# Kernel tuning notes

Measured on AMD Instinct MI355X. Metric: run time of the kernel, lower is better.

## Reference

```python
import jax, jax.numpy as jnp
import numpy as np

D = 4096  # input_dim
H = 4096  # hidden_dim


def setup_inputs() -> dict:
    key = jax.random.key(0)
    k_x, k_w, k_b, k_v, k_c = jax.random.split(key, 5)
    x = jax.random.uniform(k_x, (D, 1), dtype=jnp.float32)  # observed pixel values
    w = jax.random.normal(k_w, (H, D), dtype=jnp.float32) * 0.02
    b = jax.random.normal(k_b, (D, 1), dtype=jnp.float32) * 0.02
    v = jax.random.normal(k_v, (D, H), dtype=jnp.float32) * 0.02
    c = jax.random.normal(k_c, (H, 1), dtype=jnp.float32) * 0.02
    return {"x": x, "w": w, "b": b, "v": v, "c": c}


def reference(x, w, b, v, c):
    # Original loop: a_0 = c; a_{i+1} = a_i + w[:, i] * x[i]
    # => a_i = c + sum_{j < i} w[:, j] * x[j]  (exclusive cumsum of rank-1 updates)
    wx = w * x[:, 0][None, :]                      # [H, D]
    cum = jnp.cumsum(wx, axis=1)                   # inclusive cumsum over columns
    A = c + jnp.pad(cum[:, :-1], ((0, 0), (1, 0)))  # exclusive cumsum -> a_i in column i, [H, D]
    h = jax.nn.sigmoid(A)                          # h_i = sigmoid(a_i), [H, D]
    # p_i = sigmoid(v[i, :] @ h_i + b[i])
    logits = jnp.einsum("ih,hi->i", v, h)[:, None] + b  # [D, 1]
    p_x = jax.nn.sigmoid(logits)                   # [D, 1]
    return p_x
```

## Files before the change

### kernel.cpp

```cpp
#include <hip/hip_runtime.h>
#include <hip/hip_fp16.h>

#define D_DIM 4096
#define H_DIM 4096
#define HB 16
#define BLK 1024
#define NBLK (H_DIM / HB)
#define TILE 512
#define NTL (D_DIM / TILE)

__device__ __forceinline__ float fast_sigmoid(float a) {
    return __builtin_amdgcn_rcpf(1.0f + __expf(-a));
}

__device__ __forceinline__ float2 h2_to_f2(unsigned u) {
    union { unsigned u; __half2 h; } cvt;
    cvt.u = u;
    return __half22float2(cvt.h);
}

template <bool ATOMIC>
__global__ __launch_bounds__(BLK, 4) void nade_main_kernel(
    const float* __restrict__ x,
    const float* __restrict__ w,
    const float* __restrict__ v,
    const float* __restrict__ c,
    float* __restrict__ part)
{
    __shared__ __half S[HB][D_DIM];

    const int tid  = threadIdx.x;
    const int wv   = tid >> 6;
    const int lane = tid & 63;
    const int h0   = blockIdx.x * HB;

    const float* wrow = w + (size_t)(h0 + wv) * D_DIM + 8 * lane;
    float carry = c[h0 + wv];

    float4 wA0 = *reinterpret_cast<const float4*>(wrow + 0 * TILE);
    float4 wA1 = *reinterpret_cast<const float4*>(wrow + 0 * TILE + 4);
    float4 wB0 = *reinterpret_cast<const float4*>(wrow + 1 * TILE);
    float4 wB1 = *reinterpret_cast<const float4*>(wrow + 1 * TILE + 4);

    auto scan_tile = [&](int t, float4 w0, float4 w1) {
        const float* xp = x + t * TILE + 8 * lane;
        float4 x0 = *reinterpret_cast<const float4*>(xp);
        float4 x1 = *reinterpret_cast<const float4*>(xp + 4);
        float p0 = w0.x * x0.x, p1 = w0.y * x0.y, p2 = w0.z * x0.z, p3 = w0.w * x0.w;
        float p4 = w1.x * x1.x, p5 = w1.y * x1.y, p6 = w1.z * x1.z, p7 = w1.w * x1.w;
        float s8 = ((p0 + p1) + (p2 + p3)) + ((p4 + p5) + (p6 + p7));
        float incl = s8;
        #pragma unroll
        for (int off = 1; off < 64; off <<= 1) {
            float tv = __shfl_up(incl, off, 64);
            incl += (lane >= off) ? tv : 0.0f;
        }
        float tot = __shfl(incl, 63, 64);
        float a = carry + incl - s8;
        float sg0 = fast_sigmoid(a); a += p0;
        float sg1 = fast_sigmoid(a); a += p1;
        float sg2 = fast_sigmoid(a); a += p2;
        float sg3 = fast_sigmoid(a); a += p3;
        float sg4 = fast_sigmoid(a); a += p4;
        float sg5 = fast_sigmoid(a); a += p5;
        float sg6 = fast_sigmoid(a); a += p6;
        float sg7 = fast_sigmoid(a);
        carry += tot;
        union { __half2 h2[4]; uint4 u; } P;
        P.h2[0] = __floats2half2_rn(sg0, sg1);
        P.h2[1] = __floats2half2_rn(sg2, sg3);
        P.h2[2] = __floats2half2_rn(sg4, sg5);
        P.h2[3] = __floats2half2_rn(sg6, sg7);
        *reinterpret_cast<uint4*>(&S[wv][t * TILE + 8 * lane]) = P.u;
    };

    scan_tile(0, wA0, wA1);
    wA0 = *reinterpret_cast<const float4*>(wrow + 2 * TILE);
    wA1 = *reinterpret_cast<const float4*>(wrow + 2 * TILE + 4);
    scan_tile(1, wB0, wB1);
    wB0 = *reinterpret_cast<const float4*>(wrow + 3 * TILE);
    wB1 = *reinterpret_cast<const float4*>(wrow + 3 * TILE + 4);
    scan_tile(2, wA0, wA1);
    wA0 = *reinterpret_cast<const float4*>(wrow + 4 * TILE);
    wA1 = *reinterpret_cast<const float4*>(wrow + 4 * TILE + 4);
    scan_tile(3, wB0, wB1);
    wB0 = *reinterpret_cast<const float4*>(wrow + 5 * TILE);
    wB1 = *reinterpret_cast<const float4*>(wrow + 5 * TILE + 4);
    scan_tile(4, wA0, wA1);
    wA0 = *reinterpret_cast<const float4*>(wrow + 6 * TILE);
    wA1 = *reinterpret_cast<const float4*>(wrow + 6 * TILE + 4);
    scan_tile(5, wB0, wB1);
    wB0 = *reinterpret_cast<const float4*>(wrow + 7 * TILE);
    wB1 = *reinterpret_cast<const float4*>(wrow + 7 * TILE + 4);
    scan_tile(6, wA0, wA1);
    scan_tile(7, wB0, wB1);

    __syncthreads();

    const int i0 = 4 * tid;

    uint2 sr[16];
    #pragma unroll
    for (int h = 0; h < 16; ++h)
        sr[h] = *reinterpret_cast<const uint2*>(&S[h][i0]);

    const float* vp = v + (size_t)i0 * H_DIM + h0;
    float acc0 = 0.0f, acc1 = 0.0f, acc2 = 0.0f, acc3 = 0.0f;

    {
        float4 vr0[4], vr1[4];
        #pragma unroll
        for (int k = 0; k < 4; ++k) {
            vr0[k] = *reinterpret_cast<const float4*>(vp + 4 * k);
            vr1[k] = *reinterpret_cast<const float4*>(vp + H_DIM + 4 * k);
        }
        #pragma unroll
        for (int k = 0; k < 4; ++k) {
            float2 f0 = h2_to_f2(sr[4 * k + 0].x);
            float2 f1 = h2_to_f2(sr[4 * k + 1].x);
            float2 f2 = h2_to_f2(sr[4 * k + 2].x);
            float2 f3 = h2_to_f2(sr[4 * k + 3].x);
            acc0 += vr0[k].x * f0.x + vr0[k].y * f1.x + vr0[k].z * f2.x + vr0[k].w * f3.x;
            acc1 += vr1[k].x * f0.y + vr1[k].y * f1.y + vr1[k].z * f2.y + vr1[k].w * f3.y;
        }
    }
    {
        float4 vr2[4], vr3[4];
        #pragma unroll
        for (int k = 0; k < 4; ++k) {
            vr2[k] = *reinterpret_cast<const float4*>(vp + 2 * (size_t)H_DIM + 4 * k);
            vr3[k] = *reinterpret_cast<const float4*>(vp + 3 * (size_t)H_DIM + 4 * k);
        }
        #pragma unroll
        for (int k = 0; k < 4; ++k) {
            float2 f0 = h2_to_f2(sr[4 * k + 0].y);
            float2 f1 = h2_to_f2(sr[4 * k + 1].y);
            float2 f2 = h2_to_f2(sr[4 * k + 2].y);
            float2 f3 = h2_to_f2(sr[4 * k + 3].y);
            acc2 += vr2[k].x * f0.x + vr2[k].y * f1.x + vr2[k].z * f2.x + vr2[k].w * f3.x;
            acc3 += vr3[k].x * f0.y + vr3[k].y * f1.y + vr3[k].z * f2.y + vr3[k].w * f3.y;
        }
    }

    if (ATOMIC) {
        atomicAdd(&part[i0 + 0], acc0);
        atomicAdd(&part[i0 + 1], acc1);
        atomicAdd(&part[i0 + 2], acc2);
        atomicAdd(&part[i0 + 3], acc3);
    } else {
        float4 o; o.x = acc0; o.y = acc1; o.z = acc2; o.w = acc3;
        *reinterpret_cast<float4*>(part + (size_t)blockIdx.x * D_DIM + i0) = o;
    }
}

__global__ __launch_bounds__(1024, 1) void nade_reduce_kernel(
    const float* __restrict__ part,
    const float* __restrict__ b,
    float* __restrict__ out)
{
    __shared__ float red[16][64];
    const int tid = threadIdx.x;
    const int bg  = tid >> 6;
    const int il  = tid & 63;
    const int i   = blockIdx.x * 64 + il;
    float s = 0.0f;
    #pragma unroll
    for (int j = 0; j < NBLK / 16; ++j)
        s += part[(size_t)(bg * (NBLK / 16) + j) * D_DIM + i];
    red[bg][il] = s;
    __syncthreads();
    if (tid < 64) {
        float t = b[blockIdx.x * 64 + tid];
        #pragma unroll
        for (int j = 0; j < 16; ++j) t += red[j][tid];
        out[blockIdx.x * 64 + tid] = fast_sigmoid(t);
    }
}

__global__ __launch_bounds__(256, 1) void nade_final_atomic(
    const float* __restrict__ logits,
    const float* __restrict__ b,
    float* __restrict__ out)
{
    const int i = blockIdx.x * 256 + threadIdx.x;
    out[i] = fast_sigmoid(logits[i] + b[i]);
}

extern "C" void kernel_launch(void* const* d_in, const int* in_sizes, int n_in,
                              void* d_out, int out_size, void* d_ws, size_t ws_size,
                              hipStream_t stream)
{
    const float* x = (const float*)d_in[0];
    const float* w = (const float*)d_in[1];
    const float* b = (const float*)d_in[2];
    const float* v = (const float*)d_in[3];
    const float* c = (const float*)d_in[4];
    float* out = (float*)d_out;
    float* ws  = (float*)d_ws;

    const size_t need = (size_t)NBLK * D_DIM * sizeof(float);
    if (ws_size >= need) {
        nade_main_kernel<false><<<NBLK, BLK, 0, stream>>>(x, w, v, c, ws);
        nade_reduce_kernel<<<D_DIM / 64, 1024, 0, stream>>>(ws, b, out);
    } else {
        hipMemsetAsync(d_ws, 0, D_DIM * sizeof(float), stream);
        nade_main_kernel<true><<<NBLK, BLK, 0, stream>>>(x, w, v, c, ws);
        nade_final_atomic<<<D_DIM / 256, 256, 0, stream>>>(ws, b, out);
    }
}
```

Before: 46.98 us.

## Split fused scan+dot into separate scan, tiled v-dot, and reduce kernels

The single fused kernel is replaced by three passes. A scan kernel writes the fp16 sigmoid activations for all of H×D to global workspace. A tiled kernel then loads 128×64 slices of those activations into shared memory and dots them with v, using coalesced reads of v rows. A final kernel reduces 32 partials and applies the sigmoid. This aims to raise occupancy and parallelism beyond the 256 large 1024-thread blocks, at the cost of a 32 MB fp16 round trip through memory and an extra launch.

```diff
diff --git a/kernel.cpp b/kernel.cpp
--- a/kernel.cpp
+++ b/kernel.cpp
@@ -3,49 +3,157 @@
 
 #define D_DIM 4096
 #define H_DIM 4096
-#define HB 16
-#define BLK 1024
-#define NBLK (H_DIM / HB)
-#define TILE 512
-#define NTL (D_DIM / TILE)
 
 __device__ __forceinline__ float fast_sigmoid(float a) {
     return __builtin_amdgcn_rcpf(1.0f + __expf(-a));
 }
 
-__device__ __forceinline__ float2 h2_to_f2(unsigned u) {
-    union { unsigned u; __half2 h; } cvt;
-    cvt.u = u;
-    return __half22float2(cvt.h);
-}
-
-template <bool ATOMIC>
-__global__ __launch_bounds__(BLK, 4) void nade_main_kernel(
+__global__ __launch_bounds__(256, 4) void nade_scan_kernel(
+    const float* __restrict__ x,
+    const float* __restrict__ w,
+    const float* __restrict__ c,
+    __half* __restrict__ S)
+{
+    const int tid  = threadIdx.x;
+    const int lane = tid & 63;
+    const int h    = blockIdx.x * 4 + (tid >> 6);
+
+    const float* wrow = w + (size_t)h * D_DIM + 8 * lane;
+    __half*      srow = S + (size_t)h * D_DIM + 8 * lane;
+    float carry = c[h];
+
+    float4 wc0 = *reinterpret_cast<const float4*>(wrow);
+    float4 wc1 = *reinterpret_cast<const float4*>(wrow + 4);
+
+    #pragma unroll
+    for (int t = 0; t < 8; ++t) {
+        float4 wn0, wn1;
+        if (t < 7) {
+            wn0 = *reinterpret_cast<const float4*>(wrow + (t + 1) * 512);
+            wn1 = *reinterpret_cast<const float4*>(wrow + (t + 1) * 512 + 4);
+        }
+        float4 x0 = *reinterpret_cast<const float4*>(x + t * 512 + 8 * lane);
+        float4 x1 = *reinterpret_cast<const float4*>(x + t * 512 + 8 * lane + 4);
+
+        float p0 = wc0.x * x0.x, p1 = wc0.y * x0.y, p2 = wc0.z * x0.z, p3 = wc0.w * x0.w;
+        float p4 = wc1.x * x1.x, p5 = wc1.y * x1.y, p6 = wc1.z * x1.z, p7 = wc1.w * x1.w;
+        float s8 = ((p0 + p1) + (p2 + p3)) + ((p4 + p5) + (p6 + p7));
+        float incl = s8;
+        #pragma unroll
+        for (int off = 1; off < 64; off <<= 1) {
+            float tv = __shfl_up(incl, off, 64);
+            incl += (lane >= off) ? tv : 0.0f;
+        }
+        float tot = __shfl(incl, 63, 64);
+        float a = carry + incl - s8;
+        float sg0 = fast_sigmoid(a); a += p0;
+        float sg1 = fast_sigmoid(a); a += p1;
+        float sg2 = fast_sigmoid(a); a += p2;
+        float sg3 = fast_sigmoid(a); a += p3;
+        float sg4 = fast_sigmoid(a); a += p4;
+        float sg5 = fast_sigmoid(a); a += p5;
+        float sg6 = fast_sigmoid(a); a += p6;
+        float sg7 = fast_sigmoid(a);
+        carry += tot;
+
+        union { __half2 h2[4]; uint4 u; } P;
+        P.h2[0] = __floats2half2_rn(sg0, sg1);
+        P.h2[1] = __floats2half2_rn(sg2, sg3);
+        P.h2[2] = __floats2half2_rn(sg4, sg5);
+        P.h2[3] = __floats2half2_rn(sg6, sg7);
+        *reinterpret_cast<uint4*>(srow + t * 512) = P.u;
+
+        wc0 = wn0; wc1 = wn1;
+    }
+}
+
+__global__ __launch_bounds__(256, 8) void nade_vdot_kernel(
+    const float* __restrict__ v,
+    const __half* __restrict__ S,
+    float* __restrict__ part)
+{
+    __shared__ __half Sl[128][64];
+    __shared__ float red[4][64];
+
+    const int tid = threadIdx.x;
+    const int it  = blockIdx.x & 63;
+    const int ht  = blockIdx.x >> 6;
+    const int i0  = it * 64;
+    const int h0  = ht * 128;
+
+    {
+        const int r  = tid >> 3;
+        const int c8 = tid & 7;
+        #pragma unroll
+        for (int p = 0; p < 4; ++p) {
+            const int hh = p * 32 + r;
+            uint4 d = *reinterpret_cast<const uint4*>(
+                S + (size_t)(h0 + hh) * D_DIM + i0 + c8 * 8);
+            *reinterpret_cast<uint4*>(&Sl[hh][c8 * 8]) = d;
+        }
+    }
+    __syncthreads();
+
+    const int il = tid & 63;
+    const int q  = tid >> 6;
+    const float* vp = v + (size_t)(i0 + il) * H_DIM + h0 + q * 32;
+
+    float4 va[8];
+    #pragma unroll
+    for (int k = 0; k < 8; ++k)
+        va[k] = *reinterpret_cast<const float4*>(vp + 4 * k);
+
+    float acc = 0.0f;
+    #pragma unroll
+    for (int k = 0; k < 8; ++k) {
+        const int hb = q * 32 + 4 * k;
+        acc += va[k].x * __half2float(Sl[hb + 0][il])
+             + va[k].y * __half2float(Sl[hb + 1][il])
+             + va[k].z * __half2float(Sl[hb + 2][il])
+             + va[k].w * __half2float(Sl[hb + 3][il]);
+    }
+    red[q][il] = acc;
+    __syncthreads();
+    if (q == 0)
+        part[(size_t)ht * D_DIM + i0 + il] =
+            red[0][il] + red[1][il] + red[2][il] + red[3][il];
+}
+
+__global__ __launch_bounds__(256, 8) void nade_out_kernel(
+    const float* __restrict__ part,
+    const float* __restrict__ b,
+    float* __restrict__ out)
+{
+    const int i = blockIdx.x * 256 + threadIdx.x;
+    float t = b[i];
+    #pragma unroll
+    for (int s = 0; s < 32; ++s)
+        t += part[(size_t)s * D_DIM + i];
+    out[i] = fast_sigmoid(t);
+}
+
+__global__ __launch_bounds__(1024, 1) void nade_fused_atomic(
     const float* __restrict__ x,
     const float* __restrict__ w,
     const float* __restrict__ v,
     const float* __restrict__ c,
-    float* __restrict__ part)
-{
-    __shared__ __half S[HB][D_DIM];
+    float* __restrict__ logits)
+{
+    __shared__ __half S[16][D_DIM];
 
     const int tid  = threadIdx.x;
     const int wv   = tid >> 6;
     const int lane = tid & 63;
-    const int h0   = blockIdx.x * HB;
+    const int h0   = blockIdx.x * 16;
 
     const float* wrow = w + (size_t)(h0 + wv) * D_DIM + 8 * lane;
     float carry = c[h0 + wv];
-
-    float4 wA0 = *reinterpret_cast<const float4*>(wrow + 0 * TILE);
-    float4 wA1 = *reinterpret_cast<const float4*>(wrow + 0 * TILE + 4);
-    float4 wB0 = *reinterpret_cast<const float4*>(wrow + 1 * TILE);
-    float4 wB1 = *reinterpret_cast<const float4*>(wrow + 1 * TILE + 4);
-
-    auto scan_tile = [&](int t, float4 w0, float4 w1) {
-        const float* xp = x + t * TILE + 8 * lane;
-        float4 x0 = *reinterpret_cast<const float4*>(xp);
-        float4 x1 = *reinterpret_cast<const float4*>(xp + 4);
+    #pragma unroll
+    for (int t = 0; t < 8; ++t) {
+        float4 w0 = *reinterpret_cast<const float4*>(wrow + t * 512);
+        float4 w1 = *reinterpret_cast<const float4*>(wrow + t * 512 + 4);
+        float4 x0 = *reinterpret_cast<const float4*>(x + t * 512 + 8 * lane);
+        float4 x1 = *reinterpret_cast<const float4*>(x + t * 512 + 8 * lane + 4);
         float p0 = w0.x * x0.x, p1 = w0.y * x0.y, p2 = w0.z * x0.z, p3 = w0.w * x0.w;
         float p4 = w1.x * x1.x, p5 = w1.y * x1.y, p6 = w1.z * x1.z, p7 = w1.w * x1.w;
         float s8 = ((p0 + p1) + (p2 + p3)) + ((p4 + p5) + (p6 + p7));
@@ -71,110 +179,30 @@
         P.h2[1] = __floats2half2_rn(sg2, sg3);
         P.h2[2] = __floats2half2_rn(sg4, sg5);
         P.h2[3] = __floats2half2_rn(sg6, sg7);
-        *reinterpret_cast<uint4*>(&S[wv][t * TILE + 8 * lane]) = P.u;
-    };
-
-    scan_tile(0, wA0, wA1);
-    wA0 = *reinterpret_cast<const float4*>(wrow + 2 * TILE);
-    wA1 = *reinterpret_cast<const float4*>(wrow + 2 * TILE + 4);
-    scan_tile(1, wB0, wB1);
-    wB0 = *reinterpret_cast<const float4*>(wrow + 3 * TILE);
-    wB1 = *reinterpret_cast<const float4*>(wrow + 3 * TILE + 4);
-    scan_tile(2, wA0, wA1);
-    wA0 = *reinterpret_cast<const float4*>(wrow + 4 * TILE);
-    wA1 = *reinterpret_cast<const float4*>(wrow + 4 * TILE + 4);
-    scan_tile(3, wB0, wB1);
-    wB0 = *reinterpret_cast<const float4*>(wrow + 5 * TILE);
-    wB1 = *reinterpret_cast<const float4*>(wrow + 5 * TILE + 4);
-    scan_tile(4, wA0, wA1);
-    wA0 = *reinterpret_cast<const float4*>(wrow + 6 * TILE);
-    wA1 = *reinterpret_cast<const float4*>(wrow + 6 * TILE + 4);
-    scan_tile(5, wB0, wB1);
-    wB0 = *reinterpret_cast<const float4*>(wrow + 7 * TILE);
-    wB1 = *reinterpret_cast<const float4*>(wrow + 7 * TILE + 4);
-    scan_tile(6, wA0, wA1);
-    scan_tile(7, wB0, wB1);
-
+        *reinterpret_cast<uint4*>(&S[wv][t * 512 + 8 * lane]) = P.u;
+    }
     __syncthreads();
 
     const int i0 = 4 * tid;
-
-    uint2 sr[16];
-    #pragma unroll
-    for (int h = 0; h < 16; ++h)
-        sr[h] = *reinterpret_cast<const uint2*>(&S[h][i0]);
-
-    const float* vp = v + (size_t)i0 * H_DIM + h0;
-    float acc0 = 0.0f, acc1 = 0.0f, acc2 = 0.0f, acc3 = 0.0f;
-
-    {
-        float4 vr0[4], vr1[4];
-        #pragma unroll
-        for (int k = 0; k < 4; ++k) {
-            vr0[k] = *reinterpret_cast<const float4*>(vp + 4 * k);
-            vr1[k] = *reinterpret_cast<const float4*>(vp + H_DIM + 4 * k);
-        }
-        #pragma unroll
-        for (int k = 0; k < 4; ++k) {
-            float2 f0 = h2_to_f2(sr[4 * k + 0].x);
-            float2 f1 = h2_to_f2(sr[4 * k + 1].x);
-            float2 f2 = h2_to_f2(sr[4 * k + 2].x);
-            float2 f3 = h2_to_f2(sr[4 * k + 3].x);
-            acc0 += vr0[k].x * f0.x + vr0[k].y * f1.x + vr0[k].z * f2.x + vr0[k].w * f3.x;
-            acc1 += vr1[k].x * f0.y + vr1[k].y * f1.y + vr1[k].z * f2.y + vr1[k].w * f3.y;
-        }
-    }
-    {
-        float4 vr2[4], vr3[4];
-        #pragma unroll
-        for (int k = 0; k < 4; ++k) {
-            vr2[k] = *reinterpret_cast<const float4*>(vp + 2 * (size_t)H_DIM + 4 * k);
-            vr3[k] = *reinterpret_cast<const float4*>(vp + 3 * (size_t)H_DIM + 4 * k);
-        }
-        #pragma unroll
-        for (int k = 0; k < 4; ++k) {
-            float2 f0 = h2_to_f2(sr[4 * k + 0].y);
-            float2 f1 = h2_to_f2(sr[4 * k + 1].y);
-            float2 f2 = h2_to_f2(sr[4 * k + 2].y);
-            float2 f3 = h2_to_f2(sr[4 * k + 3].y);
-            acc2 += vr2[k].x * f0.x + vr2[k].y * f1.x + vr2[k].z * f2.x + vr2[k].w * f3.x;
-            acc3 += vr3[k].x * f0.y + vr3[k].y * f1.y + vr3[k].z * f2.y + vr3[k].w * f3.y;
-        }
-    }
-
-    if (ATOMIC) {
-        atomicAdd(&part[i0 + 0], acc0);
-        atomicAdd(&part[i0 + 1], acc1);
-        atomicAdd(&part[i0 + 2], acc2);
-        atomicAdd(&part[i0 + 3], acc3);
-    } else {
-        float4 o; o.x = acc0; o.y = acc1; o.z = acc2; o.w = acc3;
-        *reinterpret_cast<float4*>(part + (size_t)blockIdx.x * D_DIM + i0) = o;
-    }
-}
-
-__global__ __launch_bounds__(1024, 1) void nade_reduce_kernel(
-    const float* __restrict__ part,
-    const float* __restrict__ b,
-    float* __restrict__ out)
-{
-    __shared__ float red[16][64];
-    const int tid = threadIdx.x;
-    const int bg  = tid >> 6;
-    const int il  = tid & 63;
-    const int i   = blockIdx.x * 64 + il;
-    float s = 0.0f;
-    #pragma unroll
-    for (int j = 0; j < NBLK / 16; ++j)
-        s += part[(size_t)(bg * (NBLK / 16) + j) * D_DIM + i];
-    red[bg][il] = s;
-    __syncthreads();
-    if (tid < 64) {
-        float t = b[blockIdx.x * 64 + tid];
-        #pragma unroll
-        for (int j = 0; j < 16; ++j) t += red[j][tid];
-        out[blockIdx.x * 64 + tid] = fast_sigmoid(t);
-    }
+    float acc[4] = {0.f, 0.f, 0.f, 0.f};
+    #pragma unroll
+    for (int r = 0; r < 4; ++r) {
+        const float* vp = v + (size_t)(i0 + r) * H_DIM + h0;
+        float4 q0 = *reinterpret_cast<const float4*>(vp);
+        float4 q1 = *reinterpret_cast<const float4*>(vp + 4);
+        float4 q2 = *reinterpret_cast<const float4*>(vp + 8);
+        float4 q3 = *reinterpret_cast<const float4*>(vp + 12);
+        acc[r] = q0.x * __half2float(S[0][i0 + r])  + q0.y * __half2float(S[1][i0 + r])
+               + q0.z * __half2float(S[2][i0 + r])  + q0.w * __half2float(S[3][i0 + r])
+               + q1.x * __half2float(S[4][i0 + r])  + q1.y * __half2float(S[5][i0 + r])
+               + q1.z * __half2float(S[6][i0 + r])  + q1.w * __half2float(S[7][i0 + r])
+               + q2.x * __half2float(S[8][i0 + r])  + q2.y * __half2float(S[9][i0 + r])
+               + q2.z * __half2float(S[10][i0 + r]) + q2.w * __half2float(S[11][i0 + r])
+               + q3.x * __half2float(S[12][i0 + r]) + q3.y * __half2float(S[13][i0 + r])
+               + q3.z * __half2float(S[14][i0 + r]) + q3.w * __half2float(S[15][i0 + r]);
+    }
+    #pragma unroll
+    for (int r = 0; r < 4; ++r) atomicAdd(&logits[i0 + r], acc[r]);
 }
 
 __global__ __launch_bounds__(256, 1) void nade_final_atomic(
@@ -196,15 +224,20 @@
     const float* v = (const float*)d_in[3];
     const float* c = (const float*)d_in[4];
     float* out = (float*)d_out;
-    float* ws  = (float*)d_ws;
-
-    const size_t need = (size_t)NBLK * D_DIM * sizeof(float);
-    if (ws_size >= need) {
-        nade_main_kernel<false><<<NBLK, BLK, 0, stream>>>(x, w, v, c, ws);
-        nade_reduce_kernel<<<D_DIM / 64, 1024, 0, stream>>>(ws, b, out);
+
+    const size_t s_bytes    = (size_t)H_DIM * D_DIM * sizeof(__half);
+    const size_t part_bytes = (size_t)32 * D_DIM * sizeof(float);
+
+    if (ws_size >= s_bytes + part_bytes) {
+        __half* S    = (__half*)d_ws;
+        float*  part = (float*)((char*)d_ws + s_bytes);
+        nade_scan_kernel<<<H_DIM / 4, 256, 0, stream>>>(x, w, c, S);
+        nade_vdot_kernel<<<64 * 32, 256, 0, stream>>>(v, S, part);
+        nade_out_kernel<<<D_DIM / 256, 256, 0, stream>>>(part, b, out);
     } else {
-        hipMemsetAsync(d_ws, 0, D_DIM * sizeof(float), stream);
-        nade_main_kernel<true><<<NBLK, BLK, 0, stream>>>(x, w, v, c, ws);
-        nade_final_atomic<<<D_DIM / 256, 256, 0, stream>>>(ws, b, out);
-    }
-}
+        float* logits = (float*)d_ws;
+        hipMemsetAsync(logits, 0, D_DIM * sizeof(float), stream);
+        nade_fused_atomic<<<H_DIM / 16, 1024, 0, stream>>>(x, w, v, c, logits);
+        nade_final_atomic<<<D_DIM / 256, 256, 0, stream>>>(logits, b, out);
+    }
+}
```

Result: faster. 45.73 us (-2.7%).
